# Kernel tuning notes

Hardware: AMD Instinct MI355X
Metric: run time of the kernel (lower is better)

The kernel has to match this reference:

```python
import jax, jax.numpy as jnp
import numpy as np

N = 100000   # nodes
E = 1600000  # edges (avg degree 16)
D = 128      # input channels
H = 128      # hidden channels
BN_EPS = 1e-5

def setup_inputs() -> dict:
    key = jax.random.key(0)
    ks = jax.random.split(key, 8)
    x = jax.random.normal(ks[0], (N, D), dtype=jnp.float32)
    edge_index = jax.random.randint(ks[1], (2, E), 0, N, dtype=jnp.int32)
    s = 0.02
    W1 = jax.random.normal(ks[2], (D, H), dtype=jnp.float32) * s
    b1 = jnp.zeros((H,), jnp.float32)
    g1 = jnp.ones((H,), jnp.float32)   # BN gamma
    be1 = jnp.zeros((H,), jnp.float32) # BN beta
    W2 = jax.random.normal(ks[3], (H, H), dtype=jnp.float32) * s
    b2 = jnp.zeros((H,), jnp.float32)
    g2 = jnp.ones((H,), jnp.float32)
    be2 = jnp.zeros((H,), jnp.float32)
    eps = jnp.zeros((), jnp.float32)   # trainable GIN eps, init 0
    return {"x": x, "edge_index": edge_index, "W1": W1, "b1": b1, "g1": g1,
            "be1": be1, "W2": W2, "b2": b2, "g2": g2, "be2": be2, "eps": eps}

def _bn_relu(h, gamma, beta):
    # BatchNorm1d in training mode: biased batch statistics over the node dim
    mu = jnp.mean(h, axis=0)
    var = jnp.mean(jnp.square(h - mu), axis=0)
    return jax.nn.relu((h - mu) * jax.lax.rsqrt(var + BN_EPS) * gamma + beta)

def reference(x, edge_index, W1, b1, g1, be1, W2, b2, g2, be2, eps):
    src, dst = edge_index[0], edge_index[1]
    # GIN neighbor aggregation: scatter-add of source features onto destinations
    agg = jax.ops.segment_sum(x[src], dst, num_segments=x.shape[0])  # [N, D]
    h = (1.0 + eps) * x + agg
    # 2-layer MLP: Linear -> BN -> ReLU, twice
    h = _bn_relu(h @ W1 + b1, g1, be1)
    h = _bn_relu(h @ W2 + b2, g2, be2)
    return h
```

## Files before the change

### kernel.cpp

```cpp
#include <hip/hip_runtime.h>

#define DIM 128
#define BINSHIFT 7
#define BINSZ 128
#define BCAP 2560
#define EPB 8192

typedef __attribute__((ext_vector_type(8))) short bf16x8;
typedef __attribute__((ext_vector_type(4))) float f32x4;

__device__ inline unsigned short f2b(float f) {
    unsigned u = __builtin_bit_cast(unsigned, f);
    unsigned r = (u + 0x7FFFu + ((u >> 16) & 1u)) >> 16;
    return (unsigned short)r;
}
__device__ inline float b2f(unsigned short h) {
    unsigned u = ((unsigned)h) << 16;
    return __builtin_bit_cast(float, u);
}

__global__ __launch_bounds__(256)
void x_to_bf16z(const float* __restrict__ x, unsigned short* __restrict__ xb,
                unsigned* __restrict__ zbuf, int n8)
{
    if (blockIdx.x == 0) {
        #pragma unroll
        for (int q = 0; q < 6; ++q) zbuf[threadIdx.x + q * 256] = 0u;
    }
    int i = blockIdx.x * 256 + threadIdx.x;
    if (i >= n8) return;
    float4 a = ((const float4*)x)[i * 2];
    float4 b = ((const float4*)x)[i * 2 + 1];
    bf16x8 o;
    o[0] = (short)f2b(a.x); o[1] = (short)f2b(a.y); o[2] = (short)f2b(a.z); o[3] = (short)f2b(a.w);
    o[4] = (short)f2b(b.x); o[5] = (short)f2b(b.y); o[6] = (short)f2b(b.z); o[7] = (short)f2b(b.w);
    ((bf16x8*)xb)[i] = o;
}

__global__ __launch_bounds__(1024)
void bin_edges(const int* __restrict__ src, const int* __restrict__ dst,
               unsigned* __restrict__ gcur, unsigned* __restrict__ binned,
               int E, int nbins)
{
    __shared__ unsigned hist[1024];
    __shared__ unsigned base[1024];
    const int t = threadIdx.x;
    const long long bb = (long long)blockIdx.x * EPB;
    if (t < nbins) hist[t] = 0;
    __syncthreads();

    unsigned pk[8], pos[8];
    int bn[8];
    bool ok[8];
    #pragma unroll
    for (int i = 0; i < 8; ++i) {
        long long idx = bb + i * 1024 + t;
        ok[i] = idx < E;
        if (ok[i]) {
            int s = src[idx], d = dst[idx];
            pk[i] = ((unsigned)(d & (BINSZ - 1)) << 17) | (unsigned)s;
            bn[i] = d >> BINSHIFT;
            pos[i] = atomicAdd(&hist[bn[i]], 1u);
        }
    }
    __syncthreads();
    if (t < nbins) base[t] = (unsigned)t * BCAP + atomicAdd(&gcur[t], hist[t]);
    __syncthreads();
    #pragma unroll
    for (int i = 0; i < 8; ++i) {
        if (ok[i]) {
            unsigned off = base[bn[i]] + pos[i];
            if (off < (unsigned)(bn[i] + 1) * BCAP) binned[off] = pk[i];
        }
    }
}

__global__ __launch_bounds__(512)
void bin_sort(const unsigned* __restrict__ gcur, const unsigned* __restrict__ binned,
              unsigned* __restrict__ srt, unsigned* __restrict__ gbase,
              unsigned* __restrict__ ghist)
{
    __shared__ unsigned hist[BINSZ];
    __shared__ unsigned base[BINSZ];
    __shared__ unsigned cur[BINSZ];
    const int t = threadIdx.x;
    const int bin = blockIdx.x;

    if (t < BINSZ) hist[t] = 0;
    __syncthreads();

    int cnt = (int)gcur[bin];
    if (cnt > BCAP) cnt = BCAP;
    const unsigned* __restrict__ bp = binned + (size_t)bin * BCAP;

    for (int i = t; i < cnt; i += 512)
        atomicAdd(&hist[(bp[i] >> 17) & (BINSZ - 1)], 1u);
    __syncthreads();
    if (t == 0) {
        unsigned run = 0;
        for (int i = 0; i < BINSZ; ++i) { base[i] = run; run += hist[i]; }
    }
    __syncthreads();
    if (t < BINSZ) cur[t] = base[t];
    __syncthreads();
    unsigned* __restrict__ sp = srt + (size_t)bin * BCAP;
    for (int i = t; i < cnt; i += 512) {
        unsigned p = bp[i];
        unsigned pos = atomicAdd(&cur[(p >> 17) & (BINSZ - 1)], 1u);
        sp[pos] = p & 0x1FFFFu;
    }
    if (t < BINSZ) {
        gbase[bin * BINSZ + t] = base[t];
        ghist[bin * BINSZ + t] = hist[t];
    }
}

__global__ __launch_bounds__(512)
void gather_csr(const unsigned short* __restrict__ xb, const float* __restrict__ epsp,
                const unsigned* __restrict__ srt, const unsigned* __restrict__ gbase,
                const unsigned* __restrict__ ghist,
                unsigned short* __restrict__ h0b, int N)
{
    const int t = threadIdx.x;
    const int node = blockIdx.x * 32 + (t >> 4);
    if (node >= N) return;
    const int g = (t & 15) * 8;
    const float e = 1.0f + epsp[0];

    bf16x8 v0 = *(const bf16x8*)(xb + (size_t)node * DIM + g);
    float acc[8];
    #pragma unroll
    for (int q = 0; q < 8; ++q) acc[q] = e * b2f((unsigned short)v0[q]);

    const int b0 = (int)gbase[node];
    const int hn = (int)ghist[node];
    const unsigned* __restrict__ sp = srt + (size_t)(node >> BINSHIFT) * BCAP + b0;

    int j = 0;
    for (; j + 8 <= hn; j += 8) {
        unsigned s0 = sp[j+0], s1 = sp[j+1], s2 = sp[j+2], s3 = sp[j+3];
        unsigned s4 = sp[j+4], s5 = sp[j+5], s6 = sp[j+6], s7 = sp[j+7];
        bf16x8 r0 = *(const bf16x8*)(xb + (size_t)s0 * DIM + g);
        bf16x8 r1 = *(const bf16x8*)(xb + (size_t)s1 * DIM + g);
        bf16x8 r2 = *(const bf16x8*)(xb + (size_t)s2 * DIM + g);
        bf16x8 r3 = *(const bf16x8*)(xb + (size_t)s3 * DIM + g);
        bf16x8 r4 = *(const bf16x8*)(xb + (size_t)s4 * DIM + g);
        bf16x8 r5 = *(const bf16x8*)(xb + (size_t)s5 * DIM + g);
        bf16x8 r6 = *(const bf16x8*)(xb + (size_t)s6 * DIM + g);
        bf16x8 r7 = *(const bf16x8*)(xb + (size_t)s7 * DIM + g);
        #pragma unroll
        for (int q = 0; q < 8; ++q)
            acc[q] += b2f((unsigned short)r0[q]) + b2f((unsigned short)r1[q])
                    + b2f((unsigned short)r2[q]) + b2f((unsigned short)r3[q])
                    + b2f((unsigned short)r4[q]) + b2f((unsigned short)r5[q])
                    + b2f((unsigned short)r6[q]) + b2f((unsigned short)r7[q]);
    }
    for (; j + 2 <= hn; j += 2) {
        unsigned s0 = sp[j+0], s1 = sp[j+1];
        bf16x8 r0 = *(const bf16x8*)(xb + (size_t)s0 * DIM + g);
        bf16x8 r1 = *(const bf16x8*)(xb + (size_t)s1 * DIM + g);
        #pragma unroll
        for (int q = 0; q < 8; ++q)
            acc[q] += b2f((unsigned short)r0[q]) + b2f((unsigned short)r1[q]);
    }
    for (; j < hn; ++j) {
        unsigned s0 = sp[j];
        bf16x8 r0 = *(const bf16x8*)(xb + (size_t)s0 * DIM + g);
        #pragma unroll
        for (int q = 0; q < 8; ++q) acc[q] += b2f((unsigned short)r0[q]);
    }
    bf16x8 o;
    #pragma unroll
    for (int q = 0; q < 8; ++q) o[q] = (short)f2b(acc[q]);
    *(bf16x8*)(h0b + (size_t)node * DIM + g) = o;
}

template<bool APPLY_BN, bool OUT_BF16>
__global__ __launch_bounds__(1024)
void gemm_mfma(const unsigned short* __restrict__ A, const float* __restrict__ Wf,
               const float* __restrict__ bias,
               const float* __restrict__ stats_in, const float* __restrict__ gamma,
               const float* __restrict__ beta, float invN,
               void* __restrict__ outp, float* __restrict__ stats, int N)
{
    __shared__ unsigned short sWT[128 * 128];
    __shared__ float red[256];
    __shared__ float sss[256];
    const int tid = threadIdx.x;

    if (APPLY_BN && tid < 128) {
        float mu  = stats_in[tid] * invN;
        float var = fmaxf(stats_in[128 + tid] * invN - mu * mu, 0.f);
        float sc  = gamma[tid] * rsqrtf(var + 1e-5f);
        sss[tid]       = sc;
        sss[128 + tid] = beta[tid] - mu * sc;
    }
    #pragma unroll
    for (int i = 0; i < 4; ++i) {
        int idx = (i * 1024 + tid) * 4;
        float4 w = *(const float4*)&Wf[idx];
        int k = idx >> 7, n0 = idx & 127;
        sWT[(n0 + 0) * 128 + (k ^ (((n0 + 0) & 7) << 3))] = f2b(w.x);
        sWT[(n0 + 1) * 128 + (k ^ (((n0 + 1) & 7) << 3))] = f2b(w.y);
        sWT[(n0 + 2) * 128 + (k ^ (((n0 + 2) & 7) << 3))] = f2b(w.z);
        sWT[(n0 + 3) * 128 + (k ^ (((n0 + 3) & 7) << 3))] = f2b(w.w);
    }
    if (tid < 256) red[tid] = 0.f;
    __syncthreads();

    const int lane = tid & 63;
    const int wave = tid >> 6;
    const int r0   = blockIdx.x * 256 + wave * 16;
    const int rl   = lane & 15;
    const int kg   = lane >> 4;
    int rr = r0 + rl;
    int rclamp = rr < N ? rr : N - 1;
    const unsigned short* arow = A + (size_t)rclamp * DIM + kg * 8;

    f32x4 acc[8];
    #pragma unroll
    for (int nt = 0; nt < 8; ++nt) acc[nt] = (f32x4)(0.f);

    #pragma unroll
    for (int kk = 0; kk < 128; kk += 32) {
        bf16x8 a8 = *(const bf16x8*)(arow + kk);
        if (APPLY_BN) {
            const int cb = kk + kg * 8;
            bf16x8 tt;
            #pragma unroll
            for (int j = 0; j < 8; ++j) {
                float f = b2f((unsigned short)a8[j]) * sss[cb + j] + sss[128 + cb + j];
                tt[j] = (short)f2b(fmaxf(f, 0.f));
            }
            a8 = tt;
        }
        const int ks = kk + kg * 8;
        #pragma unroll
        for (int nt = 0; nt < 8; ++nt) {
            int n = nt * 16 + rl;
            bf16x8 b8 = *(const bf16x8*)&sWT[n * 128 + (ks ^ ((n & 7) << 3))];
            acc[nt] = __builtin_amdgcn_mfma_f32_16x16x32_bf16(a8, b8, acc[nt], 0, 0, 0);
        }
    }

    const int orow0 = r0 + kg * 4;
    #pragma unroll
    for (int nt = 0; nt < 8; ++nt) {
        int n = nt * 16 + rl;
        float bb = bias[n];
        float ls = 0.f, ls2 = 0.f;
        #pragma unroll
        for (int j = 0; j < 4; ++j) {
            int r = orow0 + j;
            if (r < N) {
                float v = acc[nt][j] + bb;
                if (OUT_BF16) ((unsigned short*)outp)[(size_t)r * DIM + n] = f2b(v);
                else          ((float*)outp)[(size_t)r * DIM + n] = v;
                ls += v; ls2 += v * v;
            }
        }
        ls  += __shfl_xor(ls, 16);  ls  += __shfl_xor(ls, 32);
        ls2 += __shfl_xor(ls2, 16); ls2 += __shfl_xor(ls2, 32);
        if (kg == 0) { atomicAdd(&red[n], ls); atomicAdd(&red[128 + n], ls2); }
    }
    __syncthreads();
    if (tid < 256) atomicAdd(&stats[tid], red[tid]);
}

__global__ __launch_bounds__(256)
void bn_relu_out_b(const unsigned short* __restrict__ h2b,
                   const float* __restrict__ stats, const float* __restrict__ gamma,
                   const float* __restrict__ beta, float invN,
                   float* __restrict__ out, int n8)
{
    __shared__ float sss[256];
    const int tid = threadIdx.x;
    if (tid < 128) {
        float mu  = stats[tid] * invN;
        float var = fmaxf(stats[128 + tid] * invN - mu * mu, 0.f);
        float sc  = gamma[tid] * rsqrtf(var + 1e-5f);
        sss[tid]       = sc;
        sss[128 + tid] = beta[tid] - mu * sc;
    }
    __syncthreads();
    int i = blockIdx.x * 256 + tid;
    if (i >= n8) return;
    int c = (i * 8) & 127;
    bf16x8 v = *(const bf16x8*)(h2b + (size_t)i * 8);
    float4 o0, o1;
    o0.x = fmaxf(b2f((unsigned short)v[0]) * sss[c+0] + sss[128+c+0], 0.f);
    o0.y = fmaxf(b2f((unsigned short)v[1]) * sss[c+1] + sss[128+c+1], 0.f);
    o0.z = fmaxf(b2f((unsigned short)v[2]) * sss[c+2] + sss[128+c+2], 0.f);
    o0.w = fmaxf(b2f((unsigned short)v[3]) * sss[c+3] + sss[128+c+3], 0.f);
    o1.x = fmaxf(b2f((unsigned short)v[4]) * sss[c+4] + sss[128+c+4], 0.f);
    o1.y = fmaxf(b2f((unsigned short)v[5]) * sss[c+5] + sss[128+c+5], 0.f);
    o1.z = fmaxf(b2f((unsigned short)v[6]) * sss[c+6] + sss[128+c+6], 0.f);
    o1.w = fmaxf(b2f((unsigned short)v[7]) * sss[c+7] + sss[128+c+7], 0.f);
    ((float4*)out)[i * 2 + 0] = o0;
    ((float4*)out)[i * 2 + 1] = o1;
}

extern "C" void kernel_launch(void* const* d_in, const int* in_sizes, int n_in,
                              void* d_out, int out_size, void* d_ws, size_t ws_size,
                              hipStream_t stream) {
    const float* x    = (const float*)d_in[0];
    const int*   ei   = (const int*)  d_in[1];
    const float* W1   = (const float*)d_in[2];
    const float* b1   = (const float*)d_in[3];
    const float* g1   = (const float*)d_in[4];
    const float* be1  = (const float*)d_in[5];
    const float* W2   = (const float*)d_in[6];
    const float* b2   = (const float*)d_in[7];
    const float* g2   = (const float*)d_in[8];
    const float* be2  = (const float*)d_in[9];
    const float* epsp = (const float*)d_in[10];
    float* out = (float*)d_out;

    const int N = in_sizes[0] / DIM;
    const int E = in_sizes[1] / 2;
    const int* src = ei;
    const int* dst = ei + E;
    const int nbins = (N + BINSZ - 1) >> BINSHIFT;

    const size_t SZ = (size_t)N * DIM * sizeof(unsigned short);
    char* w = (char*)d_ws;
    unsigned short* xb  = (unsigned short*)w;
    unsigned short* h0b = (unsigned short*)(w + SZ);
    unsigned short* h2b = h0b;
    unsigned short* h1b = (unsigned short*)(w + 2 * SZ);
    unsigned* binned = (unsigned*)(w + 2 * SZ);
    unsigned* srt    = binned + (size_t)nbins * BCAP;
    unsigned* gbase  = srt + (size_t)nbins * BCAP;
    unsigned* ghist  = gbase + (size_t)nbins * BINSZ;
    unsigned* gcur   = (unsigned*)(w + 3 * SZ);
    float* stats1 = (float*)(gcur + 1024);
    float* stats2 = stats1 + 256;

    const float invN = 1.0f / (float)N;
    const int n8 = N * DIM / 8;

    x_to_bf16z<<<(n8 + 255) / 256, 256, 0, stream>>>(x, xb, gcur, n8);
    bin_edges<<<(E + EPB - 1) / EPB, 1024, 0, stream>>>(src, dst, gcur, binned, E, nbins);
    bin_sort<<<nbins, 512, 0, stream>>>(gcur, binned, srt, gbase, ghist);
    gather_csr<<<(N + 31) / 32, 512, 0, stream>>>(xb, epsp, srt, gbase, ghist, h0b, N);

    const int gblocks = (N + 255) / 256;
    gemm_mfma<false, true><<<gblocks, 1024, 0, stream>>>(
        h0b, W1, b1, nullptr, nullptr, nullptr, invN, h1b, stats1, N);
    gemm_mfma<true, true><<<gblocks, 1024, 0, stream>>>(
        h1b, W2, b2, stats1, g1, be1, invN, h2b, stats2, N);
    bn_relu_out_b<<<(n8 + 255) / 256, 256, 0, stream>>>(h2b, stats2, g2, be2, invN, out, n8);
}
```

Baseline: 187.8 us.

## Fuse bin sort, neighbor aggregation and first GEMM into one per-bin kernel

Merges the bf16 cast and edge binning into a single launch, with the zeroing of counters moved to a memset. It also fuses the per-bin sort, the CSR gather and the first MFMA GEMM with its BN statistics into one kernel per 128-node bin. The sorted source list and the aggregated tile stay in shared memory, so the h0 and srt round-trips through global memory and two launches go away. The cost is much larger shared memory per block (about 75KB), which lowers occupancy, and only about 782 blocks of 512 threads for the gather-heavy phase.

```diff
diff --git a/kernel.cpp b/kernel.cpp
--- a/kernel.cpp
+++ b/kernel.cpp
@@ -19,160 +19,204 @@
     return __builtin_bit_cast(float, u);
 }
 
-__global__ __launch_bounds__(256)
-void x_to_bf16z(const float* __restrict__ x, unsigned short* __restrict__ xb,
-                unsigned* __restrict__ zbuf, int n8)
+__global__ __launch_bounds__(1024)
+void prep(const int* __restrict__ src, const int* __restrict__ dst,
+          unsigned* __restrict__ gcur, unsigned* __restrict__ binned, int E, int nbins,
+          const float* __restrict__ x, unsigned short* __restrict__ xb, int n8, int ebB)
 {
-    if (blockIdx.x == 0) {
-        #pragma unroll
-        for (int q = 0; q < 6; ++q) zbuf[threadIdx.x + q * 256] = 0u;
-    }
-    int i = blockIdx.x * 256 + threadIdx.x;
-    if (i >= n8) return;
-    float4 a = ((const float4*)x)[i * 2];
-    float4 b = ((const float4*)x)[i * 2 + 1];
-    bf16x8 o;
-    o[0] = (short)f2b(a.x); o[1] = (short)f2b(a.y); o[2] = (short)f2b(a.z); o[3] = (short)f2b(a.w);
-    o[4] = (short)f2b(b.x); o[5] = (short)f2b(b.y); o[6] = (short)f2b(b.z); o[7] = (short)f2b(b.w);
-    ((bf16x8*)xb)[i] = o;
-}
-
-__global__ __launch_bounds__(1024)
-void bin_edges(const int* __restrict__ src, const int* __restrict__ dst,
-               unsigned* __restrict__ gcur, unsigned* __restrict__ binned,
-               int E, int nbins)
+    const int t = threadIdx.x;
+    if (blockIdx.x < ebB) {
+        __shared__ unsigned hist[1024];
+        __shared__ unsigned base[1024];
+        const long long bb = (long long)blockIdx.x * EPB;
+        if (t < nbins) hist[t] = 0;
+        __syncthreads();
+
+        unsigned pk[8], pos[8];
+        int bn[8];
+        bool ok[8];
+        #pragma unroll
+        for (int i = 0; i < 8; ++i) {
+            long long idx = bb + i * 1024 + t;
+            ok[i] = idx < E;
+            if (ok[i]) {
+                int s = src[idx], d = dst[idx];
+                pk[i] = ((unsigned)(d & (BINSZ - 1)) << 17) | (unsigned)s;
+                bn[i] = d >> BINSHIFT;
+                pos[i] = atomicAdd(&hist[bn[i]], 1u);
+            }
+        }
+        __syncthreads();
+        if (t < nbins) base[t] = (unsigned)t * BCAP + atomicAdd(&gcur[t], hist[t]);
+        __syncthreads();
+        #pragma unroll
+        for (int i = 0; i < 8; ++i) {
+            if (ok[i]) {
+                unsigned off = base[bn[i]] + pos[i];
+                if (off < (unsigned)(bn[i] + 1) * BCAP) binned[off] = pk[i];
+            }
+        }
+    } else {
+        int i = (blockIdx.x - ebB) * 1024 + t;
+        if (i >= n8) return;
+        float4 a = ((const float4*)x)[i * 2];
+        float4 b = ((const float4*)x)[i * 2 + 1];
+        bf16x8 o;
+        o[0] = (short)f2b(a.x); o[1] = (short)f2b(a.y); o[2] = (short)f2b(a.z); o[3] = (short)f2b(a.w);
+        o[4] = (short)f2b(b.x); o[5] = (short)f2b(b.y); o[6] = (short)f2b(b.z); o[7] = (short)f2b(b.w);
+        ((bf16x8*)xb)[i] = o;
+    }
+}
+
+__global__ __launch_bounds__(512, 4)
+void agg_gemm1(const unsigned short* __restrict__ xb, const float* __restrict__ epsp,
+               const unsigned* __restrict__ gcur, const unsigned* __restrict__ binned,
+               const float* __restrict__ Wf, const float* __restrict__ bias,
+               unsigned short* __restrict__ h1b, float* __restrict__ stats, int N)
 {
-    __shared__ unsigned hist[1024];
-    __shared__ unsigned base[1024];
-    const int t = threadIdx.x;
-    const long long bb = (long long)blockIdx.x * EPB;
-    if (t < nbins) hist[t] = 0;
-    __syncthreads();
-
-    unsigned pk[8], pos[8];
-    int bn[8];
-    bool ok[8];
-    #pragma unroll
-    for (int i = 0; i < 8; ++i) {
-        long long idx = bb + i * 1024 + t;
-        ok[i] = idx < E;
-        if (ok[i]) {
-            int s = src[idx], d = dst[idx];
-            pk[i] = ((unsigned)(d & (BINSZ - 1)) << 17) | (unsigned)s;
-            bn[i] = d >> BINSHIFT;
-            pos[i] = atomicAdd(&hist[bn[i]], 1u);
-        }
-    }
-    __syncthreads();
-    if (t < nbins) base[t] = (unsigned)t * BCAP + atomicAdd(&gcur[t], hist[t]);
-    __syncthreads();
-    #pragma unroll
-    for (int i = 0; i < 8; ++i) {
-        if (ok[i]) {
-            unsigned off = base[bn[i]] + pos[i];
-            if (off < (unsigned)(bn[i] + 1) * BCAP) binned[off] = pk[i];
-        }
-    }
-}
-
-__global__ __launch_bounds__(512)
-void bin_sort(const unsigned* __restrict__ gcur, const unsigned* __restrict__ binned,
-              unsigned* __restrict__ srt, unsigned* __restrict__ gbase,
-              unsigned* __restrict__ ghist)
-{
-    __shared__ unsigned hist[BINSZ];
-    __shared__ unsigned base[BINSZ];
-    __shared__ unsigned cur[BINSZ];
+    __shared__ unsigned short sWT[128 * 128];
+    __shared__ unsigned short sA[128 * 128];
+    __shared__ unsigned ssrt[BCAP];
+    __shared__ unsigned hist[BINSZ], sbase[BINSZ], cur[BINSZ];
+    __shared__ float red[256];
     const int t = threadIdx.x;
     const int bin = blockIdx.x;
-
+    const int node0 = bin << BINSHIFT;
+
+    #pragma unroll
+    for (int i = 0; i < 8; ++i) {
+        int idx = (i * 512 + t) * 4;
+        float4 wv = *(const float4*)&Wf[idx];
+        int k = idx >> 7, n0 = idx & 127;
+        sWT[(n0 + 0) * 128 + (k ^ (((n0 + 0) & 7) << 3))] = f2b(wv.x);
+        sWT[(n0 + 1) * 128 + (k ^ (((n0 + 1) & 7) << 3))] = f2b(wv.y);
+        sWT[(n0 + 2) * 128 + (k ^ (((n0 + 2) & 7) << 3))] = f2b(wv.z);
+        sWT[(n0 + 3) * 128 + (k ^ (((n0 + 3) & 7) << 3))] = f2b(wv.w);
+    }
     if (t < BINSZ) hist[t] = 0;
+    if (t < 256) red[t] = 0.f;
     __syncthreads();
 
     int cnt = (int)gcur[bin];
     if (cnt > BCAP) cnt = BCAP;
     const unsigned* __restrict__ bp = binned + (size_t)bin * BCAP;
-
     for (int i = t; i < cnt; i += 512)
         atomicAdd(&hist[(bp[i] >> 17) & (BINSZ - 1)], 1u);
     __syncthreads();
     if (t == 0) {
         unsigned run = 0;
-        for (int i = 0; i < BINSZ; ++i) { base[i] = run; run += hist[i]; }
-    }
-    __syncthreads();
-    if (t < BINSZ) cur[t] = base[t];
-    __syncthreads();
-    unsigned* __restrict__ sp = srt + (size_t)bin * BCAP;
+        for (int i = 0; i < BINSZ; ++i) { sbase[i] = run; run += hist[i]; }
+    }
+    __syncthreads();
+    if (t < BINSZ) cur[t] = sbase[t];
+    __syncthreads();
     for (int i = t; i < cnt; i += 512) {
         unsigned p = bp[i];
         unsigned pos = atomicAdd(&cur[(p >> 17) & (BINSZ - 1)], 1u);
-        sp[pos] = p & 0x1FFFFu;
-    }
-    if (t < BINSZ) {
-        gbase[bin * BINSZ + t] = base[t];
-        ghist[bin * BINSZ + t] = hist[t];
-    }
-}
-
-__global__ __launch_bounds__(512)
-void gather_csr(const unsigned short* __restrict__ xb, const float* __restrict__ epsp,
-                const unsigned* __restrict__ srt, const unsigned* __restrict__ gbase,
-                const unsigned* __restrict__ ghist,
-                unsigned short* __restrict__ h0b, int N)
-{
-    const int t = threadIdx.x;
-    const int node = blockIdx.x * 32 + (t >> 4);
-    if (node >= N) return;
-    const int g = (t & 15) * 8;
+        ssrt[pos] = p & 0x1FFFFu;
+    }
+    __syncthreads();
+
     const float e = 1.0f + epsp[0];
-
-    bf16x8 v0 = *(const bf16x8*)(xb + (size_t)node * DIM + g);
-    float acc[8];
-    #pragma unroll
-    for (int q = 0; q < 8; ++q) acc[q] = e * b2f((unsigned short)v0[q]);
-
-    const int b0 = (int)gbase[node];
-    const int hn = (int)ghist[node];
-    const unsigned* __restrict__ sp = srt + (size_t)(node >> BINSHIFT) * BCAP + b0;
-
-    int j = 0;
-    for (; j + 8 <= hn; j += 8) {
-        unsigned s0 = sp[j+0], s1 = sp[j+1], s2 = sp[j+2], s3 = sp[j+3];
-        unsigned s4 = sp[j+4], s5 = sp[j+5], s6 = sp[j+6], s7 = sp[j+7];
-        bf16x8 r0 = *(const bf16x8*)(xb + (size_t)s0 * DIM + g);
-        bf16x8 r1 = *(const bf16x8*)(xb + (size_t)s1 * DIM + g);
-        bf16x8 r2 = *(const bf16x8*)(xb + (size_t)s2 * DIM + g);
-        bf16x8 r3 = *(const bf16x8*)(xb + (size_t)s3 * DIM + g);
-        bf16x8 r4 = *(const bf16x8*)(xb + (size_t)s4 * DIM + g);
-        bf16x8 r5 = *(const bf16x8*)(xb + (size_t)s5 * DIM + g);
-        bf16x8 r6 = *(const bf16x8*)(xb + (size_t)s6 * DIM + g);
-        bf16x8 r7 = *(const bf16x8*)(xb + (size_t)s7 * DIM + g);
-        #pragma unroll
-        for (int q = 0; q < 8; ++q)
-            acc[q] += b2f((unsigned short)r0[q]) + b2f((unsigned short)r1[q])
-                    + b2f((unsigned short)r2[q]) + b2f((unsigned short)r3[q])
-                    + b2f((unsigned short)r4[q]) + b2f((unsigned short)r5[q])
-                    + b2f((unsigned short)r6[q]) + b2f((unsigned short)r7[q]);
-    }
-    for (; j + 2 <= hn; j += 2) {
-        unsigned s0 = sp[j+0], s1 = sp[j+1];
-        bf16x8 r0 = *(const bf16x8*)(xb + (size_t)s0 * DIM + g);
-        bf16x8 r1 = *(const bf16x8*)(xb + (size_t)s1 * DIM + g);
-        #pragma unroll
-        for (int q = 0; q < 8; ++q)
-            acc[q] += b2f((unsigned short)r0[q]) + b2f((unsigned short)r1[q]);
-    }
-    for (; j < hn; ++j) {
-        unsigned s0 = sp[j];
-        bf16x8 r0 = *(const bf16x8*)(xb + (size_t)s0 * DIM + g);
-        #pragma unroll
-        for (int q = 0; q < 8; ++q) acc[q] += b2f((unsigned short)r0[q]);
-    }
-    bf16x8 o;
-    #pragma unroll
-    for (int q = 0; q < 8; ++q) o[q] = (short)f2b(acc[q]);
-    *(bf16x8*)(h0b + (size_t)node * DIM + g) = o;
+    const int g8 = t & 15;
+    const int g  = g8 * 8;
+    const int slot = t >> 4;
+    for (int sw = 0; sw < 4; ++sw) {
+        int dn = sw * 32 + slot;
+        int node = node0 + dn;
+        float acc[8];
+        if (node < N) {
+            bf16x8 v0 = *(const bf16x8*)(xb + (size_t)node * DIM + g);
+            #pragma unroll
+            for (int q = 0; q < 8; ++q) acc[q] = e * b2f((unsigned short)v0[q]);
+            const int b0 = (int)sbase[dn], hn = (int)hist[dn];
+            int j = 0;
+            for (; j + 8 <= hn; j += 8) {
+                unsigned s0 = ssrt[b0+j+0], s1 = ssrt[b0+j+1], s2 = ssrt[b0+j+2], s3 = ssrt[b0+j+3];
+                unsigned s4 = ssrt[b0+j+4], s5 = ssrt[b0+j+5], s6 = ssrt[b0+j+6], s7 = ssrt[b0+j+7];
+                bf16x8 r0 = *(const bf16x8*)(xb + (size_t)s0 * DIM + g);
+                bf16x8 r1 = *(const bf16x8*)(xb + (size_t)s1 * DIM + g);
+                bf16x8 r2 = *(const bf16x8*)(xb + (size_t)s2 * DIM + g);
+                bf16x8 r3 = *(const bf16x8*)(xb + (size_t)s3 * DIM + g);
+                bf16x8 r4 = *(const bf16x8*)(xb + (size_t)s4 * DIM + g);
+                bf16x8 r5 = *(const bf16x8*)(xb + (size_t)s5 * DIM + g);
+                bf16x8 r6 = *(const bf16x8*)(xb + (size_t)s6 * DIM + g);
+                bf16x8 r7 = *(const bf16x8*)(xb + (size_t)s7 * DIM + g);
+                #pragma unroll
+                for (int q = 0; q < 8; ++q)
+                    acc[q] += b2f((unsigned short)r0[q]) + b2f((unsigned short)r1[q])
+                            + b2f((unsigned short)r2[q]) + b2f((unsigned short)r3[q])
+                            + b2f((unsigned short)r4[q]) + b2f((unsigned short)r5[q])
+                            + b2f((unsigned short)r6[q]) + b2f((unsigned short)r7[q]);
+            }
+            for (; j + 2 <= hn; j += 2) {
+                unsigned s0 = ssrt[b0+j+0], s1 = ssrt[b0+j+1];
+                bf16x8 r0 = *(const bf16x8*)(xb + (size_t)s0 * DIM + g);
+                bf16x8 r1 = *(const bf16x8*)(xb + (size_t)s1 * DIM + g);
+                #pragma unroll
+                for (int q = 0; q < 8; ++q)
+                    acc[q] += b2f((unsigned short)r0[q]) + b2f((unsigned short)r1[q]);
+            }
+            for (; j < hn; ++j) {
+                unsigned s0 = ssrt[b0+j];
+                bf16x8 r0 = *(const bf16x8*)(xb + (size_t)s0 * DIM + g);
+                #pragma unroll
+                for (int q = 0; q < 8; ++q) acc[q] += b2f((unsigned short)r0[q]);
+            }
+        } else {
+            #pragma unroll
+            for (int q = 0; q < 8; ++q) acc[q] = 0.f;
+        }
+        bf16x8 o;
+        #pragma unroll
+        for (int q = 0; q < 8; ++q) o[q] = (short)f2b(acc[q]);
+        *(bf16x8*)&sA[dn * 128 + ((g8 ^ (dn & 15)) << 3)] = o;
+    }
+    __syncthreads();
+
+    const int lane = t & 63;
+    const int wave = t >> 6;
+    const int rl   = lane & 15;
+    const int kg   = lane >> 4;
+    const int r0   = wave * 16;
+
+    f32x4 acc[8];
+    #pragma unroll
+    for (int nt = 0; nt < 8; ++nt) acc[nt] = (f32x4)(0.f);
+
+    #pragma unroll
+    for (int kk = 0; kk < 4; ++kk) {
+        bf16x8 a8 = *(const bf16x8*)&sA[(r0 + rl) * 128 + (((kk * 4 + kg) ^ rl) << 3)];
+        const int ks = kk * 32 + kg * 8;
+        #pragma unroll
+        for (int nt = 0; nt < 8; ++nt) {
+            int n = nt * 16 + rl;
+            bf16x8 b8 = *(const bf16x8*)&sWT[n * 128 + (ks ^ ((n & 7) << 3))];
+            acc[nt] = __builtin_amdgcn_mfma_f32_16x16x32_bf16(a8, b8, acc[nt], 0, 0, 0);
+        }
+    }
+
+    const int orow0 = node0 + r0 + kg * 4;
+    #pragma unroll
+    for (int nt = 0; nt < 8; ++nt) {
+        int n = nt * 16 + rl;
+        float bb = bias[n];
+        float ls = 0.f, ls2 = 0.f;
+        #pragma unroll
+        for (int j = 0; j < 4; ++j) {
+            int r = orow0 + j;
+            if (r < N) {
+                float v = acc[nt][j] + bb;
+                h1b[(size_t)r * DIM + n] = f2b(v);
+                ls += v; ls2 += v * v;
+            }
+        }
+        ls  += __shfl_xor(ls, 16);  ls  += __shfl_xor(ls, 32);
+        ls2 += __shfl_xor(ls2, 16); ls2 += __shfl_xor(ls2, 32);
+        if (kg == 0) { atomicAdd(&red[n], ls); atomicAdd(&red[128 + n], ls2); }
+    }
+    __syncthreads();
+    if (t < 256) atomicAdd(&stats[t], red[t]);
 }
 
 template<bool APPLY_BN, bool OUT_BF16>
@@ -325,28 +369,22 @@
     const size_t SZ = (size_t)N * DIM * sizeof(unsigned short);
     char* w = (char*)d_ws;
     unsigned short* xb  = (unsigned short*)w;
-    unsigned short* h0b = (unsigned short*)(w + SZ);
-    unsigned short* h2b = h0b;
-    unsigned short* h1b = (unsigned short*)(w + 2 * SZ);
-    unsigned* binned = (unsigned*)(w + 2 * SZ);
-    unsigned* srt    = binned + (size_t)nbins * BCAP;
-    unsigned* gbase  = srt + (size_t)nbins * BCAP;
-    unsigned* ghist  = gbase + (size_t)nbins * BINSZ;
-    unsigned* gcur   = (unsigned*)(w + 3 * SZ);
+    unsigned short* h1b = (unsigned short*)(w + SZ);
+    unsigned* binned    = (unsigned*)(w + 2 * SZ);
+    unsigned short* h2b = (unsigned short*)(w + 2 * SZ);
+    unsigned* gcur      = (unsigned*)(w + 3 * SZ);
     float* stats1 = (float*)(gcur + 1024);
     float* stats2 = stats1 + 256;
 
     const float invN = 1.0f / (float)N;
     const int n8 = N * DIM / 8;
-
-    x_to_bf16z<<<(n8 + 255) / 256, 256, 0, stream>>>(x, xb, gcur, n8);
-    bin_edges<<<(E + EPB - 1) / EPB, 1024, 0, stream>>>(src, dst, gcur, binned, E, nbins);
-    bin_sort<<<nbins, 512, 0, stream>>>(gcur, binned, srt, gbase, ghist);
-    gather_csr<<<(N + 31) / 32, 512, 0, stream>>>(xb, epsp, srt, gbase, ghist, h0b, N);
-
+    const int ebB = (E + EPB - 1) / EPB;
+    const int castB = (n8 + 1023) / 1024;
+
+    hipMemsetAsync(gcur, 0, (1024 + 512) * sizeof(unsigned), stream);
+    prep<<<ebB + castB, 1024, 0, stream>>>(src, dst, gcur, binned, E, nbins, x, xb, n8, ebB);
+    agg_gemm1<<<nbins, 512, 0, stream>>>(xb, epsp, gcur, binned, W1, b1, h1b, stats1, N);
     const int gblocks = (N + 255) / 256;
-    gemm_mfma<false, true><<<gblocks, 1024, 0, stream>>>(
-        h0b, W1, b1, nullptr, nullptr, nullptr, invN, h1b, stats1, N);
     gemm_mfma<true, true><<<gblocks, 1024, 0, stream>>>(
         h1b, W2, b2, stats1, g1, be1, invN, h2b, stats2, N);
     bn_relu_out_b<<<(n8 + 255) / 256, 256, 0, stream>>>(h2b, stats2, g2, be2, invN, out, n8);
```

Result: faster. 179.7 us (-4.3%).
